# Optimization experiments

Measured on AMD Instinct MI355X. Metric: run time of the kernel, lower is better.

Reference implementation:

```python
import jax, jax.numpy as jnp
import numpy as np

N, T, IN, H, OUT, E = 50000, 12, 2, 128, 12, 800000


def setup_inputs() -> dict:
    key = jax.random.key(0)
    ks = jax.random.split(key, 20)
    s_in = 1.0 / np.sqrt(H)

    def w(k, shape):
        return jax.random.uniform(k, shape, jnp.float32, -s_in, s_in)

    return {
        "x": jax.random.normal(ks[0], (N, T, IN), jnp.float32),
        "edge_index": jax.random.randint(ks[1], (2, E), 0, N, dtype=jnp.int32),
        # LSTM layer 0 (input_dim -> H), gate order i,f,g,o as in PyTorch
        "Wih0": w(ks[2], (4 * H, IN)), "Whh0": w(ks[3], (4 * H, H)),
        "bih0": w(ks[4], (4 * H,)), "bhh0": w(ks[5], (4 * H,)),
        # LSTM layer 1 (H -> H)
        "Wih1": w(ks[6], (4 * H, H)), "Whh1": w(ks[7], (4 * H, H)),
        "bih1": w(ks[8], (4 * H,)), "bhh1": w(ks[9], (4 * H,)),
        # GCN layers
        "W0": w(ks[10], (H, H)), "b0": w(ks[11], (H,)),
        "W1": w(ks[12], (H, H)), "b1": w(ks[13], (H,)),
        "W2": w(ks[14], (H, OUT)), "b2": w(ks[15], (OUT,)),
    }


def _lstm_layer(seq, Wih, Whh, bih, bhh):
    # seq: [T, N, D] -> outputs [T, N, H]
    n = seq.shape[1]
    h0 = jnp.zeros((n, H), seq.dtype)
    c0 = jnp.zeros((n, H), seq.dtype)
    b = bih + bhh

    def step(carry, xt):
        h, c = carry
        z = xt @ Wih.T + h @ Whh.T + b
        i, f, g, o = jnp.split(z, 4, axis=-1)
        c = jax.nn.sigmoid(f) * c + jax.nn.sigmoid(i) * jnp.tanh(g)
        h = jax.nn.sigmoid(o) * jnp.tanh(c)
        return (h, c), h

    _, ys = jax.lax.scan(step, (h0, c0), seq)
    return ys


def _gcn(h, W, b, src, dst, norm):
    # x @ W, gather sources, edge-normalize, scatter-add to targets, + bias
    hW = h @ W
    msg = hW[src] * norm[:, None]
    return jax.ops.segment_sum(msg, dst, num_segments=N) + b


def reference(x, edge_index, Wih0, Whh0, bih0, bhh0, Wih1, Whh1, bih1, bhh1,
              W0, b0, W1, b1, W2, b2):
    # 2-layer LSTM over node time series (dropout inactive at inference)
    seq = jnp.transpose(x, (1, 0, 2))          # [T, N, IN]
    y0 = _lstm_layer(seq, Wih0, Whh0, bih0, bhh0)
    y1 = _lstm_layer(y0, Wih1, Whh1, bih1, bhh1)
    h = y1[-1]                                  # last timestep: [N, H]

    # GCN normalization with self-loops (symmetric, all edge weights 1)
    loops = jnp.arange(N, dtype=edge_index.dtype)
    src = jnp.concatenate([edge_index[0], loops])
    dst = jnp.concatenate([edge_index[1], loops])
    deg = jax.ops.segment_sum(jnp.ones(src.shape[0], h.dtype), dst, num_segments=N)
    dinv = jax.lax.rsqrt(deg)                   # deg >= 1 thanks to self-loops
    norm = dinv[src] * dinv[dst]

    h = jax.nn.relu(_gcn(h, W0, b0, src, dst, norm))
    h = jax.nn.relu(_gcn(h, W1, b1, src, dst, norm))
    out = _gcn(h, W2, b2, src, dst, norm)       # [N, OUT]
    return out
```

## Files before the change

### kernel.cpp

```cpp
#include <hip/hip_runtime.h>
#include <hip/hip_bf16.h>

#define TT 12
#define HDIM 128
#define ODIM 12
#define KS0 136
#define TPAD 36

typedef short bf16x8 __attribute__((ext_vector_type(8)));
typedef float f32x16 __attribute__((ext_vector_type(16)));

__device__ __forceinline__ float fastrcp(float x) { return __builtin_amdgcn_rcpf(x); }
__device__ __forceinline__ float sigf(float x) { return fastrcp(1.f + __expf(-x)); }
__device__ __forceinline__ float tanh_fast(float x) { return 1.f - 2.f * fastrcp(1.f + __expf(2.f * x)); }
__device__ __forceinline__ unsigned short f2bf(float f) {
    union { float f; unsigned int u; } v; v.f = f;
    unsigned int r = v.u + 0x7FFFu + ((v.u >> 16) & 1u);
    return (unsigned short)(r >> 16);
}

__global__ void pack_kernel(const float* __restrict__ Whh0, const float* __restrict__ Wih1,
                            const float* __restrict__ Whh1, unsigned short* __restrict__ Wpk)
{
    int idx = blockIdx.x * 256 + threadIdx.x;
    if (idx >= 384 * 64) return;
    int lane = idx & 63;
    int slot = idx >> 6;
    int mat = slot >> 7;
    int rem = slot & 127;
    int cb = rem >> 3, s = rem & 7;
    int col = cb * 32 + (lane & 31);
    const float* src = (mat == 0) ? Whh0 : (mat == 1) ? Wih1 : Whh1;
#pragma unroll
    for (int j = 0; j < 8; ++j) {
        int k = s * 16 + ((lane >> 5) << 3) + j;
        Wpk[((size_t)(slot * 64 + lane) << 3) + j] = f2bf(src[col * 128 + k]);
    }
}

__global__ __launch_bounds__(512, 1) void lstm_l0_kernel(
    const float* __restrict__ x,
    const unsigned short* __restrict__ Wpk,
    const float* __restrict__ Wih0,
    const float* __restrict__ bih0, const float* __restrict__ bhh0,
    unsigned short* __restrict__ h0seq,
    int N, int ntiles)
{
    __shared__ unsigned short wlds[65536];
    __shared__ unsigned short hA0[64 * KS0];
    __shared__ float xls[64 * 24];

    const int tid  = threadIdx.x;
    const int w    = tid >> 6;
    const int ln   = tid & 63;
    const int ln31 = ln & 31;
    const int half = ln >> 5;
    const int wsub = w & 3;
    const int rb   = w >> 2;
    const int col  = wsub * 32 + ln31;

    for (int i = tid * 8; i < 65536; i += 512 * 8)
        *(bf16x8*)(wlds + i) = *(const bf16x8*)(Wpk + i);

    float wx0[4], wx1[4], br0[4];
#pragma unroll
    for (int g = 0; g < 4; ++g) {
        int row = (g << 7) + col;
        wx0[g] = Wih0[row * 2 + 0];
        wx1[g] = Wih0[row * 2 + 1];
        br0[g] = bih0[row] + bhh0[row];
    }

    for (int tile = blockIdx.x; tile < ntiles; tile += gridDim.x) {
        const int nbase = tile * 64;
        __syncthreads();
        for (int i = tid; i < 64 * 24; i += 512) {
            int n = nbase + i / 24;
            xls[i] = (n < N) ? x[nbase * 24 + i] : 0.f;
        }
        for (int i = tid; i < 64 * KS0; i += 512) hA0[i] = 0;
        float c0[16];
#pragma unroll
        for (int r = 0; r < 16; ++r) c0[r] = 0.f;
        __syncthreads();

        for (int t = 0; t < TT; ++t) {
            f32x16 acc[4];
#pragma unroll
            for (int g = 0; g < 4; ++g)
#pragma unroll
                for (int e = 0; e < 16; ++e) acc[g][e] = 0.f;
#pragma unroll
            for (int s = 0; s < 8; ++s) {
                bf16x8 a = *(const bf16x8*)(hA0 + (rb * 32 + ln31) * KS0 + s * 16 + half * 8);
#pragma unroll
                for (int g = 0; g < 4; ++g) {
                    int cb = g * 4 + wsub;
                    bf16x8 b = *(const bf16x8*)(wlds + (((cb * 8 + s) * 64 + ln) << 3));
                    acc[g] = __builtin_amdgcn_mfma_f32_32x32x16_bf16(a, b, acc[g], 0, 0, 0);
                }
            }
            __syncthreads();
#pragma unroll
            for (int r = 0; r < 16; ++r) {
                int node = rb * 32 + (r & 3) + 8 * (r >> 2) + 4 * half;
                float xa = xls[node * 24 + t * 2 + 0];
                float xb = xls[node * 24 + t * 2 + 1];
                float zi = acc[0][r] + br0[0] + wx0[0] * xa + wx1[0] * xb;
                float zf = acc[1][r] + br0[1] + wx0[1] * xa + wx1[1] * xb;
                float zg = acc[2][r] + br0[2] + wx0[2] * xa + wx1[2] * xb;
                float zo = acc[3][r] + br0[3] + wx0[3] * xa + wx1[3] * xb;
                float cn = sigf(zf) * c0[r] + sigf(zi) * tanh_fast(zg);
                c0[r] = cn;
                float h = sigf(zo) * tanh_fast(cn);
                unsigned short us = f2bf(h);
                hA0[node * KS0 + col] = us;
                int n = nbase + node;
                if (n < N) h0seq[(n * TT + t) * HDIM + col] = us;
            }
            __syncthreads();
        }
    }
}

__global__ __launch_bounds__(256, 1) void lstm_l1f_kernel(
    const unsigned short* __restrict__ h0seq,
    const unsigned short* __restrict__ Wpk,
    const float* __restrict__ bih1, const float* __restrict__ bhh1,
    float* __restrict__ hbuf,
    int N, int ntiles)
{
    __shared__ unsigned short wlds[65536];
    __shared__ unsigned short hA1[64 * KS0];

    const int tid  = threadIdx.x;
    const int w    = tid >> 6;
    const int ln   = tid & 63;
    const int ln31 = ln & 31;
    const int half = ln >> 5;
    const int ch   = w * 32 + ln31;

    for (int i = tid * 8; i < 65536; i += 256 * 8)
        *(bf16x8*)(wlds + i) = *(const bf16x8*)(Wpk + 131072 + i);

    bf16x8 wfr[4][8];
#pragma unroll
    for (int g = 0; g < 4; ++g)
#pragma unroll
        for (int s = 0; s < 8; ++s) {
            int cb = g * 4 + w;
            wfr[g][s] = *(const bf16x8*)(Wpk + 65536 + (((cb * 8 + s) * 64 + ln) << 3));
        }

    float br1[4];
#pragma unroll
    for (int g = 0; g < 4; ++g) {
        int row = (g << 7) + ch;
        br1[g] = bih1[row] + bhh1[row];
    }

    const bf16x8 zv = {0, 0, 0, 0, 0, 0, 0, 0};
    __syncthreads();

    for (int tile = blockIdx.x; tile < ntiles; tile += gridDim.x) {
        __syncthreads();
        for (int i = tid; i < 64 * KS0; i += 256) hA1[i] = 0;
        float c1[2][16];
#pragma unroll
        for (int rb = 0; rb < 2; ++rb)
#pragma unroll
            for (int r = 0; r < 16; ++r) c1[rb][r] = 0.f;
        __syncthreads();

        const int na0 = tile * 64 + ln31;
        const int na1 = na0 + 32;
        const bool ok0 = na0 < N, ok1 = na1 < N;

        for (int t = 0; t < TT; ++t) {
            bf16x8 a0[2][8];
#pragma unroll
            for (int s = 0; s < 8; ++s) {
                a0[0][s] = ok0 ? __builtin_nontemporal_load(
                    (const bf16x8*)(h0seq + ((size_t)na0 * TT + t) * HDIM + s * 16 + half * 8)) : zv;
                a0[1][s] = ok1 ? __builtin_nontemporal_load(
                    (const bf16x8*)(h0seq + ((size_t)na1 * TT + t) * HDIM + s * 16 + half * 8)) : zv;
            }

            f32x16 acc[2][4];
#pragma unroll
            for (int rb = 0; rb < 2; ++rb)
#pragma unroll
                for (int g = 0; g < 4; ++g)
#pragma unroll
                    for (int e = 0; e < 16; ++e) acc[rb][g][e] = 0.f;

#pragma unroll
            for (int s = 0; s < 8; ++s) {
                bf16x8 a1[2];
#pragma unroll
                for (int rb = 0; rb < 2; ++rb)
                    a1[rb] = *(const bf16x8*)(hA1 + (rb * 32 + ln31) * KS0 + s * 16 + half * 8);
#pragma unroll
                for (int g = 0; g < 4; ++g) {
                    int cb = g * 4 + w;
                    bf16x8 b = *(const bf16x8*)(wlds + (((cb * 8 + s) * 64 + ln) << 3));
#pragma unroll
                    for (int rb = 0; rb < 2; ++rb)
                        acc[rb][g] = __builtin_amdgcn_mfma_f32_32x32x16_bf16(a1[rb], b, acc[rb][g], 0, 0, 0);
                }
            }
#pragma unroll
            for (int s = 0; s < 8; ++s)
#pragma unroll
                for (int g = 0; g < 4; ++g)
#pragma unroll
                    for (int rb = 0; rb < 2; ++rb)
                        acc[rb][g] = __builtin_amdgcn_mfma_f32_32x32x16_bf16(a0[rb][s], wfr[g][s], acc[rb][g], 0, 0, 0);
            __syncthreads();

#pragma unroll
            for (int rb = 0; rb < 2; ++rb) {
#pragma unroll
                for (int r = 0; r < 16; ++r) {
                    int rr = rb * 32 + (r & 3) + 8 * (r >> 2) + 4 * half;
                    float zi = acc[rb][0][r] + br1[0];
                    float zf = acc[rb][1][r] + br1[1];
                    float zg = acc[rb][2][r] + br1[2];
                    float zo = acc[rb][3][r] + br1[3];
                    float cn = sigf(zf) * c1[rb][r] + sigf(zi) * tanh_fast(zg);
                    c1[rb][r] = cn;
                    float h = sigf(zo) * tanh_fast(cn);
                    if (t + 1 < TT) {
                        hA1[rr * KS0 + ch] = f2bf(h);
                    } else {
                        int n = tile * 64 + rr;
                        if (n < N) hbuf[n * HDIM + ch] = h;
                    }
                }
            }
            __syncthreads();
        }
    }
}

__global__ void deg_count_kernel(const int* __restrict__ ei, int* __restrict__ degi, int E)
{
    int e = blockIdx.x * 256 + threadIdx.x;
    if (e < E) atomicAdd(&degi[ei[E + e]], 1);
}

__global__ void row_alloc_kernel(const int* __restrict__ degi, int* __restrict__ row_ptr,
                                 float* __restrict__ dinv, int* __restrict__ counter, int N)
{
    int n = blockIdx.x * 256 + threadIdx.x;
    int lane = threadIdx.x & 63;
    int v = (n < N) ? degi[n] : 0;
    int incl = v;
    for (int off = 1; off < 64; off <<= 1) {
        int u = __shfl_up(incl, off);
        if (lane >= off) incl += u;
    }
    int base = 0;
    if (lane == 63) base = atomicAdd(counter, incl);
    base = __shfl(base, 63);
    if (n < N) {
        row_ptr[n] = base + (incl - v);
        dinv[n] = rsqrtf((float)(v + 1));
    }
}

__global__ void csr_fill_kernel(const int* __restrict__ ei, const int* __restrict__ row_ptr,
                                int* __restrict__ fill, int* __restrict__ csr_src, int E)
{
    int e = blockIdx.x * 256 + threadIdx.x;
    if (e < E) {
        int d = ei[E + e];
        int p = atomicAdd(&fill[d], 1);
        csr_src[row_ptr[d] + p] = ei[e];
    }
}

__global__ __launch_bounds__(256) void gemm128_kernel(const float* __restrict__ X,
                                                      const float* __restrict__ W,
                                                      float* __restrict__ Y, int N)
{
    __shared__ float XT[128 * TPAD];
    const int tid = threadIdx.x;
    const int nbase = blockIdx.x * 32;
    for (int idx = tid; idx < 32 * 128; idx += 256) {
        int m = idx >> 7, k = idx & 127;
        int n = nbase + m;
        XT[k * TPAD + m] = (n < N) ? X[n * HDIM + k] : 0.f;
    }
    __syncthreads();
    const int c  = tid & 63;
    const int mb = (tid >> 6) << 3;
    float acc[8][2];
#pragma unroll
    for (int i = 0; i < 8; ++i) { acc[i][0] = 0.f; acc[i][1] = 0.f; }
    for (int k = 0; k < 128; ++k) {
        const float* xr = &XT[k * TPAD + mb];
        float4 a0 = *(const float4*)(xr);
        float4 a1 = *(const float4*)(xr + 4);
        float a[8] = {a0.x, a0.y, a0.z, a0.w, a1.x, a1.y, a1.z, a1.w};
        float b0 = W[k * HDIM + c];
        float b1 = W[k * HDIM + c + 64];
#pragma unroll
        for (int i = 0; i < 8; ++i) {
            acc[i][0] = fmaf(a[i], b0, acc[i][0]);
            acc[i][1] = fmaf(a[i], b1, acc[i][1]);
        }
    }
#pragma unroll
    for (int i = 0; i < 8; ++i) {
        int n = nbase + mb + i;
        if (n < N) {
            Y[n * HDIM + c]      = acc[i][0];
            Y[n * HDIM + c + 64] = acc[i][1];
        }
    }
}

__global__ void gemm12_kernel(const float* __restrict__ X, const float* __restrict__ W2,
                              float* __restrict__ Y, int N)
{
    int idx = blockIdx.x * 256 + threadIdx.x;
    int n = idx / ODIM, c = idx - n * ODIM;
    if (n >= N) return;
    float acc = 0.f;
    for (int k = 0; k < 128; ++k) acc = fmaf(X[n * HDIM + k], W2[k * ODIM + c], acc);
    Y[n * ODIM + c] = acc;
}

__global__ __launch_bounds__(128) void agg128_kernel(const float* __restrict__ hW,
        const int* __restrict__ row_ptr, const int* __restrict__ degi,
        const int* __restrict__ csr_src, const float* __restrict__ dinv,
        const float* __restrict__ bias, float* __restrict__ out, int N, int do_relu)
{
    int n = blockIdx.x;
    int c = threadIdx.x;
    float dn = dinv[n];
    float acc = hW[n * HDIM + c] * dn * dn;
    int start = row_ptr[n];
    int cnt = degi[n];
    for (int i = 0; i < cnt; ++i) {
        int s = csr_src[start + i];
        acc = fmaf(hW[s * HDIM + c], dinv[s] * dn, acc);
    }
    float v = acc + bias[c];
    if (do_relu) v = fmaxf(v, 0.f);
    out[n * HDIM + c] = v;
}

__global__ void agg12_kernel(const float* __restrict__ hW, const int* __restrict__ row_ptr,
        const int* __restrict__ degi, const int* __restrict__ csr_src,
        const float* __restrict__ dinv, const float* __restrict__ b2,
        float* __restrict__ out, int N)
{
    int idx = blockIdx.x * 256 + threadIdx.x;
    int n = idx / ODIM, c = idx - n * ODIM;
    if (n >= N) return;
    float dn = dinv[n];
    float acc = hW[n * ODIM + c] * dn * dn;
    int start = row_ptr[n], cnt = degi[n];
    for (int i = 0; i < cnt; ++i) {
        int s = csr_src[start + i];
        acc = fmaf(hW[s * ODIM + c], dinv[s] * dn, acc);
    }
    out[n * ODIM + c] = acc + b2[c];
}

extern "C" void kernel_launch(void* const* d_in, const int* in_sizes, int n_in,
                              void* d_out, int out_size, void* d_ws, size_t ws_size,
                              hipStream_t stream)
{
    const float* x     = (const float*)d_in[0];
    const int*   ei    = (const int*)d_in[1];
    const float* Wih0  = (const float*)d_in[2];
    const float* Whh0  = (const float*)d_in[3];
    const float* bih0  = (const float*)d_in[4];
    const float* bhh0  = (const float*)d_in[5];
    const float* Wih1  = (const float*)d_in[6];
    const float* Whh1  = (const float*)d_in[7];
    const float* bih1  = (const float*)d_in[8];
    const float* bhh1  = (const float*)d_in[9];
    const float* W0    = (const float*)d_in[10];
    const float* b0    = (const float*)d_in[11];
    const float* W1    = (const float*)d_in[12];
    const float* b1    = (const float*)d_in[13];
    const float* W2    = (const float*)d_in[14];
    const float* b2    = (const float*)d_in[15];
    float* out = (float*)d_out;

    const int N = in_sizes[0] / (TT * 2);
    const int E = in_sizes[1] / 2;

    unsigned short* Wpk = (unsigned short*)d_ws;
    float* fbase = (float*)((char*)d_ws + 393216);
    float* hbuf = fbase;
    float* buf1 = hbuf + (size_t)N * HDIM;
    float* buf2 = buf1 + (size_t)N * HDIM;
    float* dinv = buf2 + (size_t)N * HDIM;
    int* degi    = (int*)(dinv + N);
    int* fill    = degi + N;
    int* counter = fill + N;
    int* row_ptr = counter + 1;
    int* csr_src = row_ptr + N;
    size_t h0_off = (((size_t)((char*)(csr_src + E) - (char*)d_ws)) + 255) & ~(size_t)255;
    unsigned short* h0seq = (unsigned short*)((char*)d_ws + h0_off);

    hipMemsetAsync(degi, 0, (size_t)(2 * N + 1) * sizeof(int), stream);

    pack_kernel<<<(384 * 64 + 255) / 256, 256, 0, stream>>>(Whh0, Wih1, Whh1, Wpk);

    const int ntiles = (N + 63) / 64;
    lstm_l0_kernel<<<256, 512, 0, stream>>>(x, Wpk, Wih0, bih0, bhh0, h0seq, N, ntiles);
    lstm_l1f_kernel<<<256, 256, 0, stream>>>(h0seq, Wpk, bih1, bhh1, hbuf, N, ntiles);

    deg_count_kernel<<<(E + 255) / 256, 256, 0, stream>>>(ei, degi, E);
    row_alloc_kernel<<<(N + 255) / 256, 256, 0, stream>>>(degi, row_ptr, dinv, counter, N);
    csr_fill_kernel<<<(E + 255) / 256, 256, 0, stream>>>(ei, row_ptr, fill, csr_src, E);

    gemm128_kernel<<<(N + 31) / 32, 256, 0, stream>>>(hbuf, W0, buf1, N);
    agg128_kernel<<<N, 128, 0, stream>>>(buf1, row_ptr, degi, csr_src, dinv, b0, buf2, N, 1);
    gemm128_kernel<<<(N + 31) / 32, 256, 0, stream>>>(buf2, W1, buf1, N);
    agg128_kernel<<<N, 128, 0, stream>>>(buf1, row_ptr, degi, csr_src, dinv, b1, buf2, N, 1);
    gemm12_kernel<<<((size_t)N * ODIM + 255) / 256, 256, 0, stream>>>(buf2, W2, buf1, N);
    agg12_kernel<<<((size_t)N * ODIM + 255) / 256, 256, 0, stream>>>(
        buf1, row_ptr, degi, csr_src, dinv, b2, out, N);
}
```

Baseline: 1.134 ms.

## Retile LSTM layer-1 to 16x16 MFMA with 8 waves and store GCN features in fp16

Layer-1 LSTM kernel moves from 4 waves of 32x32x16 MFMA to 8 waves of 16x16x32 MFMA. Weights for Wih1/Whh1 are repacked for the new fragment layout, and the h0seq loads are interleaved per k-slice instead of preloaded. Separately, the GCN transformed features (hW) are stored as fp16, which halves the gather bandwidth in the aggregation kernels. The cost is fp16 rounding of the messages and higher register pressure from the larger block.

```diff
diff --git a/kernel.cpp b/kernel.cpp
--- a/kernel.cpp
+++ b/kernel.cpp
@@ -9,6 +9,7 @@
 
 typedef short bf16x8 __attribute__((ext_vector_type(8)));
 typedef float f32x16 __attribute__((ext_vector_type(16)));
+typedef float f32x4  __attribute__((ext_vector_type(4)));
 
 __device__ __forceinline__ float fastrcp(float x) { return __builtin_amdgcn_rcpf(x); }
 __device__ __forceinline__ float sigf(float x) { return fastrcp(1.f + __expf(-x)); }
@@ -28,13 +29,23 @@
     int slot = idx >> 6;
     int mat = slot >> 7;
     int rem = slot & 127;
-    int cb = rem >> 3, s = rem & 7;
-    int col = cb * 32 + (lane & 31);
-    const float* src = (mat == 0) ? Whh0 : (mat == 1) ? Wih1 : Whh1;
-#pragma unroll
-    for (int j = 0; j < 8; ++j) {
-        int k = s * 16 + ((lane >> 5) << 3) + j;
-        Wpk[((size_t)(slot * 64 + lane) << 3) + j] = f2bf(src[col * 128 + k]);
+    if (mat == 0) {
+        int cb = rem >> 3, s = rem & 7;
+        int col = cb * 32 + (lane & 31);
+#pragma unroll
+        for (int j = 0; j < 8; ++j) {
+            int k = s * 16 + ((lane >> 5) << 3) + j;
+            Wpk[((size_t)(slot * 64 + lane) << 3) + j] = f2bf(Whh0[col * 128 + k]);
+        }
+    } else {
+        const float* src = (mat == 1) ? Wih1 : Whh1;
+        int ct = rem >> 2, ks = rem & 3;
+        int col = ct * 16 + (lane & 15);
+#pragma unroll
+        for (int j = 0; j < 8; ++j) {
+            int k = ks * 32 + ((lane >> 4) << 3) + j;
+            Wpk[((size_t)(slot * 64 + lane) << 3) + j] = f2bf(src[col * 128 + k]);
+        }
     }
 }
 
@@ -123,7 +134,7 @@
     }
 }
 
-__global__ __launch_bounds__(256, 1) void lstm_l1f_kernel(
+__global__ __launch_bounds__(512) void lstm_l1f_kernel(
     const unsigned short* __restrict__ h0seq,
     const unsigned short* __restrict__ Wpk,
     const float* __restrict__ bih1, const float* __restrict__ bhh1,
@@ -136,20 +147,20 @@
     const int tid  = threadIdx.x;
     const int w    = tid >> 6;
     const int ln   = tid & 63;
-    const int ln31 = ln & 31;
-    const int half = ln >> 5;
-    const int ch   = w * 32 + ln31;
-
-    for (int i = tid * 8; i < 65536; i += 256 * 8)
+    const int l15  = ln & 15;
+    const int quad = ln >> 4;
+    const int ch   = w * 16 + l15;
+
+    for (int i = tid * 8; i < 65536; i += 512 * 8)
         *(bf16x8*)(wlds + i) = *(const bf16x8*)(Wpk + 131072 + i);
 
-    bf16x8 wfr[4][8];
+    bf16x8 wfr[4][4];
 #pragma unroll
     for (int g = 0; g < 4; ++g)
 #pragma unroll
-        for (int s = 0; s < 8; ++s) {
-            int cb = g * 4 + w;
-            wfr[g][s] = *(const bf16x8*)(Wpk + 65536 + (((cb * 8 + s) * 64 + ln) << 3));
+        for (int ks = 0; ks < 4; ++ks) {
+            int slot = (g * 8 + w) * 4 + ks;
+            wfr[g][ks] = *(const bf16x8*)(Wpk + 65536 + ((size_t)(slot * 64 + ln) << 3));
         }
 
     float br1[4];
@@ -164,76 +175,72 @@
 
     for (int tile = blockIdx.x; tile < ntiles; tile += gridDim.x) {
         __syncthreads();
-        for (int i = tid; i < 64 * KS0; i += 256) hA1[i] = 0;
-        float c1[2][16];
-#pragma unroll
-        for (int rb = 0; rb < 2; ++rb)
-#pragma unroll
-            for (int r = 0; r < 16; ++r) c1[rb][r] = 0.f;
+        for (int i = tid; i < 64 * KS0; i += 512) hA1[i] = 0;
+        float c1[16];
+#pragma unroll
+        for (int r = 0; r < 16; ++r) c1[r] = 0.f;
         __syncthreads();
 
-        const int na0 = tile * 64 + ln31;
-        const int na1 = na0 + 32;
-        const bool ok0 = na0 < N, ok1 = na1 < N;
-
         for (int t = 0; t < TT; ++t) {
-            bf16x8 a0[2][8];
-#pragma unroll
-            for (int s = 0; s < 8; ++s) {
-                a0[0][s] = ok0 ? __builtin_nontemporal_load(
-                    (const bf16x8*)(h0seq + ((size_t)na0 * TT + t) * HDIM + s * 16 + half * 8)) : zv;
-                a0[1][s] = ok1 ? __builtin_nontemporal_load(
-                    (const bf16x8*)(h0seq + ((size_t)na1 * TT + t) * HDIM + s * 16 + half * 8)) : zv;
+            f32x4 acc[4][4];
+#pragma unroll
+            for (int rt = 0; rt < 4; ++rt)
+#pragma unroll
+                for (int g = 0; g < 4; ++g)
+#pragma unroll
+                    for (int e = 0; e < 4; ++e) acc[rt][g][e] = 0.f;
+
+#pragma unroll
+            for (int ks = 0; ks < 4; ++ks) {
+                bf16x8 a[4];
+#pragma unroll
+                for (int rt = 0; rt < 4; ++rt) {
+                    int n = tile * 64 + rt * 16 + l15;
+                    a[rt] = (n < N)
+                        ? __builtin_nontemporal_load(
+                            (const bf16x8*)(h0seq + ((size_t)n * TT + t) * HDIM + ks * 32 + quad * 8))
+                        : zv;
+                }
+#pragma unroll
+                for (int g = 0; g < 4; ++g)
+#pragma unroll
+                    for (int rt = 0; rt < 4; ++rt)
+                        acc[rt][g] = __builtin_amdgcn_mfma_f32_16x16x32_bf16(a[rt], wfr[g][ks], acc[rt][g], 0, 0, 0);
             }
-
-            f32x16 acc[2][4];
-#pragma unroll
-            for (int rb = 0; rb < 2; ++rb)
-#pragma unroll
-                for (int g = 0; g < 4; ++g)
-#pragma unroll
-                    for (int e = 0; e < 16; ++e) acc[rb][g][e] = 0.f;
-
-#pragma unroll
-            for (int s = 0; s < 8; ++s) {
-                bf16x8 a1[2];
-#pragma unroll
-                for (int rb = 0; rb < 2; ++rb)
-                    a1[rb] = *(const bf16x8*)(hA1 + (rb * 32 + ln31) * KS0 + s * 16 + half * 8);
+#pragma unroll
+            for (int ks = 0; ks < 4; ++ks) {
+                bf16x8 a[4];
+#pragma unroll
+                for (int rt = 0; rt < 4; ++rt)
+                    a[rt] = *(const bf16x8*)(hA1 + (rt * 16 + l15) * KS0 + ks * 32 + quad * 8);
 #pragma unroll
                 for (int g = 0; g < 4; ++g) {
-                    int cb = g * 4 + w;
-                    bf16x8 b = *(const bf16x8*)(wlds + (((cb * 8 + s) * 64 + ln) << 3));
-#pragma unroll
-                    for (int rb = 0; rb < 2; ++rb)
-                        acc[rb][g] = __builtin_amdgcn_mfma_f32_32x32x16_bf16(a1[rb], b, acc[rb][g], 0, 0, 0);
+                    int slot = (g * 8 + w) * 4 + ks;
+                    bf16x8 b = *(const bf16x8*)(wlds + ((size_t)(slot * 64 + ln) << 3));
+#pragma unroll
+                    for (int rt = 0; rt < 4; ++rt)
+                        acc[rt][g] = __builtin_amdgcn_mfma_f32_16x16x32_bf16(a[rt], b, acc[rt][g], 0, 0, 0);
                 }
             }
-#pragma unroll
-            for (int s = 0; s < 8; ++s)
-#pragma unroll
-                for (int g = 0; g < 4; ++g)
-#pragma unroll
-                    for (int rb = 0; rb < 2; ++rb)
-                        acc[rb][g] = __builtin_amdgcn_mfma_f32_32x32x16_bf16(a0[rb][s], wfr[g][s], acc[rb][g], 0, 0, 0);
             __syncthreads();
 
 #pragma unroll
-            for (int rb = 0; rb < 2; ++rb) {
-#pragma unroll
-                for (int r = 0; r < 16; ++r) {
-                    int rr = rb * 32 + (r & 3) + 8 * (r >> 2) + 4 * half;
-                    float zi = acc[rb][0][r] + br1[0];
-                    float zf = acc[rb][1][r] + br1[1];
-                    float zg = acc[rb][2][r] + br1[2];
-                    float zo = acc[rb][3][r] + br1[3];
-                    float cn = sigf(zf) * c1[rb][r] + sigf(zi) * tanh_fast(zg);
-                    c1[rb][r] = cn;
+            for (int rt = 0; rt < 4; ++rt) {
+#pragma unroll
+                for (int rg = 0; rg < 4; ++rg) {
+                    int ci = rt * 4 + rg;
+                    float zi = acc[rt][0][rg] + br1[0];
+                    float zf = acc[rt][1][rg] + br1[1];
+                    float zg = acc[rt][2][rg] + br1[2];
+                    float zo = acc[rt][3][rg] + br1[3];
+                    float cn = sigf(zf) * c1[ci] + sigf(zi) * tanh_fast(zg);
+                    c1[ci] = cn;
                     float h = sigf(zo) * tanh_fast(cn);
+                    int nd = rt * 16 + quad * 4 + rg;
                     if (t + 1 < TT) {
-                        hA1[rr * KS0 + ch] = f2bf(h);
+                        hA1[nd * KS0 + ch] = f2bf(h);
                     } else {
-                        int n = tile * 64 + rr;
+                        int n = tile * 64 + nd;
                         if (n < N) hbuf[n * HDIM + ch] = h;
                     }
                 }
@@ -282,7 +289,7 @@
 
 __global__ __launch_bounds__(256) void gemm128_kernel(const float* __restrict__ X,
                                                       const float* __restrict__ W,
-                                                      float* __restrict__ Y, int N)
+                                                      _Float16* __restrict__ Y, int N)
 {
     __shared__ float XT[128 * TPAD];
     const int tid = threadIdx.x;
@@ -315,24 +322,24 @@
     for (int i = 0; i < 8; ++i) {
         int n = nbase + mb + i;
         if (n < N) {
-            Y[n * HDIM + c]      = acc[i][0];
-            Y[n * HDIM + c + 64] = acc[i][1];
+            Y[n * HDIM + c]      = (_Float16)acc[i][0];
+            Y[n * HDIM + c + 64] = (_Float16)acc[i][1];
         }
     }
 }
 
 __global__ void gemm12_kernel(const float* __restrict__ X, const float* __restrict__ W2,
-                              float* __restrict__ Y, int N)
+                              _Float16* __restrict__ Y, int N)
 {
     int idx = blockIdx.x * 256 + threadIdx.x;
     int n = idx / ODIM, c = idx - n * ODIM;
     if (n >= N) return;
     float acc = 0.f;
     for (int k = 0; k < 128; ++k) acc = fmaf(X[n * HDIM + k], W2[k * ODIM + c], acc);
-    Y[n * ODIM + c] = acc;
-}
-
-__global__ __launch_bounds__(128) void agg128_kernel(const float* __restrict__ hW,
+    Y[n * ODIM + c] = (_Float16)acc;
+}
+
+__global__ __launch_bounds__(128) void agg128_kernel(const _Float16* __restrict__ hW,
         const int* __restrict__ row_ptr, const int* __restrict__ degi,
         const int* __restrict__ csr_src, const float* __restrict__ dinv,
         const float* __restrict__ bias, float* __restrict__ out, int N, int do_relu)
@@ -340,19 +347,19 @@
     int n = blockIdx.x;
     int c = threadIdx.x;
     float dn = dinv[n];
-    float acc = hW[n * HDIM + c] * dn * dn;
+    float acc = (float)hW[n * HDIM + c] * dn * dn;
     int start = row_ptr[n];
     int cnt = degi[n];
     for (int i = 0; i < cnt; ++i) {
         int s = csr_src[start + i];
-        acc = fmaf(hW[s * HDIM + c], dinv[s] * dn, acc);
+        acc = fmaf((float)hW[s * HDIM + c], dinv[s] * dn, acc);
     }
     float v = acc + bias[c];
     if (do_relu) v = fmaxf(v, 0.f);
     out[n * HDIM + c] = v;
 }
 
-__global__ void agg12_kernel(const float* __restrict__ hW, const int* __restrict__ row_ptr,
+__global__ void agg12_kernel(const _Float16* __restrict__ hW, const int* __restrict__ row_ptr,
         const int* __restrict__ degi, const int* __restrict__ csr_src,
         const float* __restrict__ dinv, const float* __restrict__ b2,
         float* __restrict__ out, int N)
@@ -361,11 +368,11 @@
     int n = idx / ODIM, c = idx - n * ODIM;
     if (n >= N) return;
     float dn = dinv[n];
-    float acc = hW[n * ODIM + c] * dn * dn;
+    float acc = (float)hW[n * ODIM + c] * dn * dn;
     int start = row_ptr[n], cnt = degi[n];
     for (int i = 0; i < cnt; ++i) {
         int s = csr_src[start + i];
-        acc = fmaf(hW[s * ODIM + c], dinv[s] * dn, acc);
+        acc = fmaf((float)hW[s * ODIM + c], dinv[s] * dn, acc);
     }
     out[n * ODIM + c] = acc + b2[c];
 }
@@ -408,6 +415,7 @@
     int* csr_src = row_ptr + N;
     size_t h0_off = (((size_t)((char*)(csr_src + E) - (char*)d_ws)) + 255) & ~(size_t)255;
     unsigned short* h0seq = (unsigned short*)((char*)d_ws + h0_off);
+    _Float16* buf1h = (_Float16*)buf1;
 
     hipMemsetAsync(degi, 0, (size_t)(2 * N + 1) * sizeof(int), stream);
 
@@ -415,17 +423,17 @@
 
     const int ntiles = (N + 63) / 64;
     lstm_l0_kernel<<<256, 512, 0, stream>>>(x, Wpk, Wih0, bih0, bhh0, h0seq, N, ntiles);
-    lstm_l1f_kernel<<<256, 256, 0, stream>>>(h0seq, Wpk, bih1, bhh1, hbuf, N, ntiles);
+    lstm_l1f_kernel<<<256, 512, 0, stream>>>(h0seq, Wpk, bih1, bhh1, hbuf, N, ntiles);
 
     deg_count_kernel<<<(E + 255) / 256, 256, 0, stream>>>(ei, degi, E);
     row_alloc_kernel<<<(N + 255) / 256, 256, 0, stream>>>(degi, row_ptr, dinv, counter, N);
     csr_fill_kernel<<<(E + 255) / 256, 256, 0, stream>>>(ei, row_ptr, fill, csr_src, E);
 
-    gemm128_kernel<<<(N + 31) / 32, 256, 0, stream>>>(hbuf, W0, buf1, N);
-    agg128_kernel<<<N, 128, 0, stream>>>(buf1, row_ptr, degi, csr_src, dinv, b0, buf2, N, 1);
-    gemm128_kernel<<<(N + 31) / 32, 256, 0, stream>>>(buf2, W1, buf1, N);
-    agg128_kernel<<<N, 128, 0, stream>>>(buf1, row_ptr, degi, csr_src, dinv, b1, buf2, N, 1);
-    gemm12_kernel<<<((size_t)N * ODIM + 255) / 256, 256, 0, stream>>>(buf2, W2, buf1, N);
+    gemm128_kernel<<<(N + 31) / 32, 256, 0, stream>>>(hbuf, W0, buf1h, N);
+    agg128_kernel<<<N, 128, 0, stream>>>(buf1h, row_ptr, degi, csr_src, dinv, b0, buf2, N, 1);
+    gemm128_kernel<<<(N + 31) / 32, 256, 0, stream>>>(buf2, W1, buf1h, N);
+    agg128_kernel<<<N, 128, 0, stream>>>(buf1h, row_ptr, degi, csr_src, dinv, b1, buf2, N, 1);
+    gemm12_kernel<<<((size_t)N * ODIM + 255) / 256, 256, 0, stream>>>(buf2, W2, buf1h, N);
     agg12_kernel<<<((size_t)N * ODIM + 255) / 256, 256, 0, stream>>>(
-        buf1, row_ptr, degi, csr_src, dinv, b2, out, N);
-}
+        buf1h, row_ptr, degi, csr_src, dinv, b2, out, N);
+}
```

Result: faster. 1.068 ms (-5.8%).
